# Optimization experiments

Hardware: AMD Instinct MI355X
Metric: run time of the kernel (lower is better)

Reference implementation:

```python
import jax, jax.numpy as jnp
import numpy as np

MAX_WORDS = 2048  # max word tokens per sequence (static num_segments)


def setup_inputs() -> dict:
    key = jax.random.key(0)
    k1, k2, k3, k4 = jax.random.split(key, 4)
    B, S, H, D = 8, 4096, 768, 1024
    embeddings = jax.random.normal(k1, (B, S, H), dtype=jnp.float32)
    proj_w = jax.random.normal(k2, (H, D), dtype=jnp.float32) * 0.02
    proj_b = jax.random.normal(k3, (D,), dtype=jnp.float32) * 0.02
    masks = jnp.ones((B, S), dtype=jnp.int32)
    word_ids = jnp.sort(jax.random.randint(k4, (B, S), 0, MAX_WORDS), axis=-1)
    return {"embeddings": embeddings, "proj_w": proj_w, "proj_b": proj_b,
            "masks": masks, "word_ids": word_ids}


def reference(embeddings, proj_w, proj_b, masks, word_ids):
    B, S, H = embeddings.shape
    W = MAX_WORDS
    # Flatten batch+word into one segment id space: seg in [0, B*W)
    seg = (word_ids + jnp.arange(B, dtype=word_ids.dtype)[:, None] * W).reshape(-1)
    flat_emb = embeddings.reshape(B * S, H)
    # segment-sum of embeddings over subwords of each word  -> (B, W, H)
    sum_emb = jax.ops.segment_sum(flat_emb, seg, num_segments=B * W).reshape(B, W, H)
    ones = jnp.ones((B * S,), dtype=jnp.float32)
    counts = jax.ops.segment_sum(ones, seg, num_segments=B * W).reshape(B, W)
    mcounts = jax.ops.segment_sum(masks.reshape(-1).astype(jnp.float32), seg,
                                  num_segments=B * W).reshape(B, W)
    # word is valid iff it has >=1 subword and ALL its subwords have mask==1
    valid = (counts > 0) & (counts == mcounts)
    mean_emb = sum_emb / jnp.maximum(counts, 1.0)[..., None]
    token_embeddings = jnp.where(valid[..., None], mean_emb, 0.0)  # (B, W, H)
    token_masks = valid.astype(jnp.int32)                          # (B, W)
    # projection: hidden 768 -> config.hidden_size 1024
    out = jnp.einsum('bwh,hd->bwd', token_embeddings, proj_w) + proj_b
    return out, token_masks
```

## Files before the change

### kernel.cpp

```cpp
#include <hip/hip_runtime.h>
#include <hip/hip_bf16.h>
#include <stdint.h>

#define Bn 8
#define Sn 4096
#define Hn 768
#define Dn 1024
#define Wn 2048

typedef __attribute__((ext_vector_type(8))) short short8;
typedef __attribute__((ext_vector_type(4))) short short4v;
typedef __attribute__((ext_vector_type(4))) float floatx4;

__device__ __forceinline__ void load_lds16(const void* g, void* l) {
  __builtin_amdgcn_global_load_lds(
      (const __attribute__((address_space(1))) void*)g,
      (__attribute__((address_space(3))) void*)l, 16, 0, 0);
}

__global__ __launch_bounds__(256) void k_prep(const float* __restrict__ pw,
                                              const int* __restrict__ wid,
                                              __hip_bfloat16* __restrict__ wb,
                                              int* __restrict__ starts) {
  if (blockIdx.x < 768) {
    __shared__ float tile[32][33];
    const int bt = blockIdx.x;
    const int d0 = (bt % 32) * 32, h0 = (bt / 32) * 32;
    const int tx = threadIdx.x & 31, ty = threadIdx.x >> 5;
#pragma unroll
    for (int i = 0; i < 32; i += 8)
      tile[ty + i][tx] = pw[(size_t)(h0 + ty + i) * Dn + d0 + tx];
    __syncthreads();
#pragma unroll
    for (int i = 0; i < 32; i += 8)
      wb[(size_t)(d0 + ty + i) * Hn + h0 + tx] = (__hip_bfloat16)tile[tx][ty + i];
  } else {
    const int bid = blockIdx.x - 768;
    const int g = bid * 256 + threadIdx.x;
    const int b = g >> 12, s = g & (Sn - 1);
    const int* wbi = wid + (size_t)b * Sn;
    int* sb = starts + b * (Wn + 1);
    const int cur = wbi[s];
    const int prev = (s == 0) ? -1 : wbi[s - 1];
    for (int ww = prev + 1; ww <= cur; ++ww) sb[ww] = s;
    if (s == Sn - 1)
      for (int ww = cur + 1; ww <= Wn; ++ww) sb[ww] = Sn;
  }
}

__global__ __launch_bounds__(256) void k_words(const float* __restrict__ emb,
                                               const int* __restrict__ masks,
                                               const int* __restrict__ starts,
                                               __hip_bfloat16* __restrict__ wa,
                                               float* __restrict__ out_masks) {
  const int b = blockIdx.y;
  const int wave = threadIdx.x >> 6, lane = threadIdx.x & 63;
  const int w = blockIdx.x * 4 + wave;

  const int* sb = starts + b * (Wn + 1);
  const int start = sb[w];
  const int end = sb[w + 1];
  const int count = end - start;

  const int* mb = masks + (size_t)b * Sn;
  bool allone = true;
  for (int s0 = start; s0 < end; s0 += 64) {
    const int idx = s0 + lane;
    allone = allone && ((idx < end) ? (mb[idx] == 1) : true);
  }
  const bool valid = (count > 0) && __all(allone);
  const float inv = valid ? 1.0f / (float)count : 0.0f;

  floatx4 sum[3] = {{0.f, 0.f, 0.f, 0.f}, {0.f, 0.f, 0.f, 0.f}, {0.f, 0.f, 0.f, 0.f}};
  const float* eb = emb + (size_t)b * Sn * Hn;
  int s = start;
  for (; s + 1 < end; s += 2) {
    const floatx4* r0 = (const floatx4*)(eb + (size_t)s * Hn);
    const floatx4* r1 = (const floatx4*)(eb + (size_t)(s + 1) * Hn);
#pragma unroll
    for (int j = 0; j < 3; ++j) sum[j] += r0[j * 64 + lane];
#pragma unroll
    for (int j = 0; j < 3; ++j) sum[j] += r1[j * 64 + lane];
  }
  if (s < end) {
    const floatx4* r0 = (const floatx4*)(eb + (size_t)s * Hn);
#pragma unroll
    for (int j = 0; j < 3; ++j) sum[j] += r0[j * 64 + lane];
  }

  const size_t rowbase = ((size_t)b * Wn + w) * Hn;
#pragma unroll
  for (int j = 0; j < 3; ++j) {
    short4v o;
#pragma unroll
    for (int c = 0; c < 4; ++c) {
      __hip_bfloat16 h = (__hip_bfloat16)(sum[j][c] * inv);
      o[c] = *reinterpret_cast<short*>(&h);
    }
    *(short4v*)&wa[rowbase + (size_t)(j * 64 + lane) * 4] = o;
  }
  if (lane == 0) out_masks[(size_t)b * Wn + w] = valid ? 1.0f : 0.0f;
}

__global__ __launch_bounds__(256) void k_gemm(const short* __restrict__ A,
                                              const short* __restrict__ Bt,
                                              const float* __restrict__ bias,
                                              float* __restrict__ out) {
  constexpr int K = Hn;
  constexpr int N = Dn;
  __shared__ __align__(16) short lsA[2][128 * 32];
  __shared__ __align__(16) short lsB[2][128 * 32];

  const int t = threadIdx.x;
  const int lane = t & 63, wave = t >> 6;
  const int wm = wave >> 1, wn = wave & 1;
  const int lane16 = lane & 15, quad = lane >> 4;

  const int linear = blockIdx.x;
  const int xcd = linear & 7;
  const int o = linear >> 3;
  const int m0 = (xcd * 16 + (o >> 3)) * 128;
  const int n0 = (o & 7) * 128;

  const int lrow = t >> 2;
  const int lcol = (t & 3) * 8;
  const short* gA0 = A + (size_t)(m0 + lrow) * K + lcol;
  const short* gB0 = Bt + (size_t)(n0 + lrow) * K + lcol;
  const int loff = lrow * 32 + lcol;

  float bv[4];
#pragma unroll
  for (int ni = 0; ni < 4; ++ni)
    bv[ni] = bias[n0 + wn * 64 + ni * 16 + lane16];

  floatx4 acc[4][4];
#pragma unroll
  for (int i = 0; i < 4; ++i)
#pragma unroll
    for (int j = 0; j < 4; ++j) acc[i][j] = (floatx4){0.f, 0.f, 0.f, 0.f};

  for (int k0 = 0; k0 < K; k0 += 64) {
    load_lds16(gA0 + k0,                    &lsA[0][loff]);
    load_lds16(gA0 + (size_t)64 * K + k0,   &lsA[0][loff + 64 * 32]);
    load_lds16(gA0 + k0 + 32,               &lsA[1][loff]);
    load_lds16(gA0 + (size_t)64 * K + k0 + 32, &lsA[1][loff + 64 * 32]);
    load_lds16(gB0 + k0,                    &lsB[0][loff]);
    load_lds16(gB0 + (size_t)64 * K + k0,   &lsB[0][loff + 64 * 32]);
    load_lds16(gB0 + k0 + 32,               &lsB[1][loff]);
    load_lds16(gB0 + (size_t)64 * K + k0 + 32, &lsB[1][loff + 64 * 32]);
    __syncthreads();

#pragma unroll
    for (int sp = 0; sp < 2; ++sp) {
      short8 af[4], bf[4];
#pragma unroll
      for (int mi = 0; mi < 4; ++mi)
        af[mi] = *(const short8*)&lsA[sp][(wm * 64 + mi * 16 + lane16) * 32 + quad * 8];
#pragma unroll
      for (int ni = 0; ni < 4; ++ni)
        bf[ni] = *(const short8*)&lsB[sp][(wn * 64 + ni * 16 + lane16) * 32 + quad * 8];

#pragma unroll
      for (int mi = 0; mi < 4; ++mi)
#pragma unroll
        for (int ni = 0; ni < 4; ++ni)
          acc[mi][ni] = __builtin_amdgcn_mfma_f32_16x16x32_bf16(af[mi], bf[ni], acc[mi][ni], 0, 0, 0);
    }
    __syncthreads();
  }

#pragma unroll
  for (int mi = 0; mi < 4; ++mi) {
#pragma unroll
    for (int ni = 0; ni < 4; ++ni) {
      const int n = n0 + wn * 64 + ni * 16 + lane16;
#pragma unroll
      for (int r = 0; r < 4; ++r) {
        const int m = m0 + wm * 64 + mi * 16 + quad * 4 + r;
        out[(size_t)m * N + n] = acc[mi][ni][r] + bv[ni];
      }
    }
  }
}

extern "C" void kernel_launch(void* const* d_in, const int* in_sizes, int n_in,
                              void* d_out, int out_size, void* d_ws, size_t ws_size,
                              hipStream_t stream) {
  const float* emb    = (const float*)d_in[0];
  const float* proj_w = (const float*)d_in[1];
  const float* proj_b = (const float*)d_in[2];
  const int*   masks  = (const int*)d_in[3];
  const int*   wid    = (const int*)d_in[4];

  float* out = (float*)d_out;
  float* out_masks = out + (size_t)Bn * Wn * Dn;

  __hip_bfloat16* wb = (__hip_bfloat16*)d_ws;
  __hip_bfloat16* wa = wb + (size_t)Dn * Hn;
  int* starts = (int*)(wa + (size_t)Bn * Wn * Hn);

  k_prep<<<dim3(768 + (Bn * Sn) / 256), 256, 0, stream>>>(proj_w, wid, wb, starts);

  k_words<<<dim3(Wn / 4, Bn), 256, 0, stream>>>(emb, masks, starts, wa, out_masks);

  k_gemm<<<dim3(1024), 256, 0, stream>>>((const short*)wa, (const short*)wb, proj_b, out);
}
```

Measured before the change: 206.9 us.

## Restructure GEMM into 256x128 tiles with triple-buffered swizzled LDS pipeline

Replaces the simple 128x128 double-pass GEMM with a 512-thread, 256x128 tile kernel that keeps a three-slot LDS ring buffer (144 KB dynamic shared memory) and prefetches two K-steps ahead. LDS rows are XOR-swizzled to avoid bank conflicts, and MFMA issue is split into two halves with s_setprio and explicit waitcnt/barriers so global loads overlap compute. The aim is to hide memory latency and raise MFMA utilisation. In exchange, occupancy is limited by the large LDS footprint, the grid halves to 512 blocks, and hand-placed waitcnts make the schedule fragile.

```diff
diff --git a/kernel.cpp b/kernel.cpp
--- a/kernel.cpp
+++ b/kernel.cpp
@@ -102,72 +102,131 @@
   if (lane == 0) out_masks[(size_t)b * Wn + w] = valid ? 1.0f : 0.0f;
 }
 
-__global__ __launch_bounds__(256) void k_gemm(const short* __restrict__ A,
-                                              const short* __restrict__ Bt,
-                                              const float* __restrict__ bias,
-                                              float* __restrict__ out) {
-  constexpr int K = Hn;
-  constexpr int N = Dn;
-  __shared__ __align__(16) short lsA[2][128 * 32];
-  __shared__ __align__(16) short lsB[2][128 * 32];
+constexpr int GK = Hn;
+constexpr int LDS_A = 256 * 64;
+constexpr int LDS_B = 128 * 64;
+constexpr int LDS_T = LDS_A + LDS_B;
+
+__global__ __launch_bounds__(512, 2) void k_gemm(const short* __restrict__ A,
+                                                 const short* __restrict__ Bt,
+                                                 const float* __restrict__ bias,
+                                                 float* __restrict__ out) {
+  extern __shared__ __align__(16) short ls[];
 
   const int t = threadIdx.x;
-  const int lane = t & 63, wave = t >> 6;
+  const int lane = t & 63;
+  const int wave = t >> 6;
   const int wm = wave >> 1, wn = wave & 1;
   const int lane16 = lane & 15, quad = lane >> 4;
+  const int swz = lane16 & 7;
 
   const int linear = blockIdx.x;
   const int xcd = linear & 7;
   const int o = linear >> 3;
-  const int m0 = (xcd * 16 + (o >> 3)) * 128;
+  const int m0 = (xcd * 8 + (o >> 3)) * 256;
   const int n0 = (o & 7) * 128;
 
-  const int lrow = t >> 2;
-  const int lcol = (t & 3) * 8;
-  const short* gA0 = A + (size_t)(m0 + lrow) * K + lcol;
-  const short* gB0 = Bt + (size_t)(n0 + lrow) * K + lcol;
-  const int loff = lrow * 32 + lcol;
+  const int rA = t >> 3;
+  const int ssw = ((t & 7) ^ (rA & 7)) * 8;
+  const short* gAs = A + (size_t)(m0 + rA) * GK + ssw;
+  const short* gBs = Bt + (size_t)(n0 + rA) * GK + ssw;
+
+  auto stage_a3 = [&](int slot, int tt) {
+    short* d = ls + slot * LDS_T + t * 8;
+    const short* g = gAs + tt * 64;
+    load_lds16(g, d);
+    load_lds16(g + (size_t)64 * GK, d + 4096);
+    load_lds16(g + (size_t)128 * GK, d + 8192);
+  };
+  auto stage_b3 = [&](int slot, int tt) {
+    short* d = ls + slot * LDS_T + t * 8;
+    load_lds16(gAs + tt * 64 + (size_t)192 * GK, d + 12288);
+    load_lds16(gBs + tt * 64, d + 16384);
+    load_lds16(gBs + tt * 64 + (size_t)64 * GK, d + 20480);
+  };
+
+  auto ld_af = [&](short8 (&af)[2][2], int mib, const short* bufA) {
+#pragma unroll
+    for (int m2 = 0; m2 < 2; ++m2)
+#pragma unroll
+      for (int ks = 0; ks < 2; ++ks)
+        af[m2][ks] = *(const short8*)&bufA[(wm * 64 + (mib + m2) * 16 + lane16) * 64 +
+                                           ((((ks << 2) | quad) ^ swz) << 3)];
+  };
+  auto ld_bf = [&](short8 (&bf)[4][2], const short* bufB) {
+#pragma unroll
+    for (int ni = 0; ni < 4; ++ni)
+#pragma unroll
+      for (int ks = 0; ks < 2; ++ks)
+        bf[ni][ks] = *(const short8*)&bufB[(wn * 64 + ni * 16 + lane16) * 64 +
+                                           ((((ks << 2) | quad) ^ swz) << 3)];
+  };
+
+  floatx4 acc[4][4];
+#pragma unroll
+  for (int i = 0; i < 4; ++i)
+#pragma unroll
+    for (int j = 0; j < 4; ++j) acc[i][j] = (floatx4){0.f, 0.f, 0.f, 0.f};
+
+  auto mmac2 = [&](short8 (&af)[2][2], short8 (&bf)[4][2], int mib) {
+    __builtin_amdgcn_s_setprio(1);
+#pragma unroll
+    for (int m2 = 0; m2 < 2; ++m2)
+#pragma unroll
+      for (int ni = 0; ni < 4; ++ni)
+#pragma unroll
+        for (int ks = 0; ks < 2; ++ks)
+          acc[mib + m2][ni] = __builtin_amdgcn_mfma_f32_16x16x32_bf16(
+              af[m2][ks], bf[ni][ks], acc[mib + m2][ni], 0, 0, 0);
+    __builtin_amdgcn_s_setprio(0);
+  };
+
+  stage_a3(0, 0);
+  stage_b3(0, 0);
+  stage_a3(1, 1);
+  stage_b3(1, 1);
+  asm volatile("s_waitcnt vmcnt(6)" ::: "memory");
+  __builtin_amdgcn_sched_barrier(0);
+  __builtin_amdgcn_s_barrier();
+
+  int cur = 0;
+#pragma unroll 1
+  for (int tt = 0; tt < 12; ++tt) {
+    const short* bufA = ls + cur * LDS_T;
+    const short* bufB = bufA + LDS_A;
+    const int nx2 = (cur + 2 >= 3) ? cur - 1 : cur + 2;
+    const bool st = tt < 10;
+    short8 af[2][2], bf[4][2];
+
+    ld_af(af, 0, bufA);
+    ld_bf(bf, bufB);
+    if (st) stage_a3(nx2, tt + 2);
+    __builtin_amdgcn_s_barrier();
+    asm volatile("s_waitcnt lgkmcnt(0)" ::: "memory");
+    __builtin_amdgcn_sched_barrier(0);
+    mmac2(af, bf, 0);
+    __builtin_amdgcn_s_barrier();
+
+    ld_af(af, 2, bufA);
+    if (st) stage_b3(nx2, tt + 2);
+    if (tt < 10) {
+      asm volatile("s_waitcnt vmcnt(6)" ::: "memory");
+    } else if (tt == 10) {
+      asm volatile("s_waitcnt vmcnt(0)" ::: "memory");
+    }
+    __builtin_amdgcn_sched_barrier(0);
+    __builtin_amdgcn_s_barrier();
+    asm volatile("s_waitcnt lgkmcnt(0)" ::: "memory");
+    __builtin_amdgcn_sched_barrier(0);
+    mmac2(af, bf, 2);
+    __builtin_amdgcn_s_barrier();
+
+    cur = (cur + 1 == 3) ? 0 : cur + 1;
+  }
 
   float bv[4];
 #pragma unroll
-  for (int ni = 0; ni < 4; ++ni)
-    bv[ni] = bias[n0 + wn * 64 + ni * 16 + lane16];
-
-  floatx4 acc[4][4];
-#pragma unroll
-  for (int i = 0; i < 4; ++i)
-#pragma unroll
-    for (int j = 0; j < 4; ++j) acc[i][j] = (floatx4){0.f, 0.f, 0.f, 0.f};
-
-  for (int k0 = 0; k0 < K; k0 += 64) {
-    load_lds16(gA0 + k0,                    &lsA[0][loff]);
-    load_lds16(gA0 + (size_t)64 * K + k0,   &lsA[0][loff + 64 * 32]);
-    load_lds16(gA0 + k0 + 32,               &lsA[1][loff]);
-    load_lds16(gA0 + (size_t)64 * K + k0 + 32, &lsA[1][loff + 64 * 32]);
-    load_lds16(gB0 + k0,                    &lsB[0][loff]);
-    load_lds16(gB0 + (size_t)64 * K + k0,   &lsB[0][loff + 64 * 32]);
-    load_lds16(gB0 + k0 + 32,               &lsB[1][loff]);
-    load_lds16(gB0 + (size_t)64 * K + k0 + 32, &lsB[1][loff + 64 * 32]);
-    __syncthreads();
-
-#pragma unroll
-    for (int sp = 0; sp < 2; ++sp) {
-      short8 af[4], bf[4];
-#pragma unroll
-      for (int mi = 0; mi < 4; ++mi)
-        af[mi] = *(const short8*)&lsA[sp][(wm * 64 + mi * 16 + lane16) * 32 + quad * 8];
-#pragma unroll
-      for (int ni = 0; ni < 4; ++ni)
-        bf[ni] = *(const short8*)&lsB[sp][(wn * 64 + ni * 16 + lane16) * 32 + quad * 8];
-
-#pragma unroll
-      for (int mi = 0; mi < 4; ++mi)
-#pragma unroll
-        for (int ni = 0; ni < 4; ++ni)
-          acc[mi][ni] = __builtin_amdgcn_mfma_f32_16x16x32_bf16(af[mi], bf[ni], acc[mi][ni], 0, 0, 0);
-    }
-    __syncthreads();
-  }
+  for (int ni = 0; ni < 4; ++ni) bv[ni] = bias[n0 + wn * 64 + ni * 16 + lane16];
 
 #pragma unroll
   for (int mi = 0; mi < 4; ++mi) {
@@ -177,7 +236,7 @@
 #pragma unroll
       for (int r = 0; r < 4; ++r) {
         const int m = m0 + wm * 64 + mi * 16 + quad * 4 + r;
-        out[(size_t)m * N + n] = acc[mi][ni][r] + bv[ni];
+        out[(size_t)m * Dn + n] = acc[mi][ni][r] + bv[ni];
       }
     }
   }
@@ -203,5 +262,10 @@
 
   k_words<<<dim3(Wn / 4, Bn), 256, 0, stream>>>(emb, masks, starts, wa, out_masks);
 
-  k_gemm<<<dim3(1024), 256, 0, stream>>>((const short*)wa, (const short*)wb, proj_b, out);
-}
+  constexpr int kGemmLds = 3 * LDS_T * (int)sizeof(short);
+  static_assert(kGemmLds == 147456, "LDS budget");
+  (void)hipFuncSetAttribute((const void*)k_gemm,
+                            hipFuncAttributeMaxDynamicSharedMemorySize, kGemmLds);
+  k_gemm<<<dim3(512), 512, kGemmLds, stream>>>((const short*)wa, (const short*)wb,
+                                               proj_b, out);
+}
```

Result: no change. 209.9 us (+1.5%).

## Fuse prep and word kernels using wave-level binary search for word bounds

Applied to the files above, without the earlier changes.

Replaces the separate starts-table build and word-averaging kernels with one front kernel. Each wave finds its word's start and end by a two-level ballot/popcount lower-bound search over the sorted word ids, and the weight transpose runs as extra blocks in the same launch. This removes one launch and its dependency, plus the starts buffer round trip. The GEMM output also switches to nontemporal stores to reduce cache pollution. Each wave now does extra index loads for the search.

```diff
diff --git a/kernel.cpp b/kernel.cpp
--- a/kernel.cpp
+++ b/kernel.cpp
@@ -18,13 +18,27 @@
       (__attribute__((address_space(3))) void*)l, 16, 0, 0);
 }
 
-__global__ __launch_bounds__(256) void k_prep(const float* __restrict__ pw,
-                                              const int* __restrict__ wid,
-                                              __hip_bfloat16* __restrict__ wb,
-                                              int* __restrict__ starts) {
-  if (blockIdx.x < 768) {
+__device__ __forceinline__ int lb4096(const int* __restrict__ a, int x, int lane) {
+  const int p = a[lane << 6];
+  const unsigned long long m1 = __ballot(p < x);
+  const int n1 = __popcll(m1);
+  const int base = (n1 > 0 ? n1 - 1 : 0) << 6;
+  const int q = a[base + lane];
+  const unsigned long long m2 = __ballot(q < x);
+  return base + __popcll(m2);
+}
+
+__global__ __launch_bounds__(256) void k_front(const float* __restrict__ emb,
+                                               const float* __restrict__ pw,
+                                               const int* __restrict__ masks,
+                                               const int* __restrict__ wid,
+                                               __hip_bfloat16* __restrict__ wb,
+                                               __hip_bfloat16* __restrict__ wa,
+                                               float* __restrict__ out_masks) {
+  const int bid = blockIdx.x;
+  if (bid >= 4096) {
     __shared__ float tile[32][33];
-    const int bt = blockIdx.x;
+    const int bt = bid - 4096;
     const int d0 = (bt % 32) * 32, h0 = (bt / 32) * 32;
     const int tx = threadIdx.x & 31, ty = threadIdx.x >> 5;
 #pragma unroll
@@ -34,32 +48,16 @@
 #pragma unroll
     for (int i = 0; i < 32; i += 8)
       wb[(size_t)(d0 + ty + i) * Hn + h0 + tx] = (__hip_bfloat16)tile[tx][ty + i];
-  } else {
-    const int bid = blockIdx.x - 768;
-    const int g = bid * 256 + threadIdx.x;
-    const int b = g >> 12, s = g & (Sn - 1);
-    const int* wbi = wid + (size_t)b * Sn;
-    int* sb = starts + b * (Wn + 1);
-    const int cur = wbi[s];
-    const int prev = (s == 0) ? -1 : wbi[s - 1];
-    for (int ww = prev + 1; ww <= cur; ++ww) sb[ww] = s;
-    if (s == Sn - 1)
-      for (int ww = cur + 1; ww <= Wn; ++ww) sb[ww] = Sn;
-  }
-}
-
-__global__ __launch_bounds__(256) void k_words(const float* __restrict__ emb,
-                                               const int* __restrict__ masks,
-                                               const int* __restrict__ starts,
-                                               __hip_bfloat16* __restrict__ wa,
-                                               float* __restrict__ out_masks) {
-  const int b = blockIdx.y;
+    return;
+  }
+
+  const int b = bid >> 9;
   const int wave = threadIdx.x >> 6, lane = threadIdx.x & 63;
-  const int w = blockIdx.x * 4 + wave;
-
-  const int* sb = starts + b * (Wn + 1);
-  const int start = sb[w];
-  const int end = sb[w + 1];
+  const int w = (bid & 511) * 4 + wave;
+
+  const int* wbi = wid + (size_t)b * Sn;
+  const int start = lb4096(wbi, w, lane);
+  const int end = lb4096(wbi, w + 1, lane);
   const int count = end - start;
 
   const int* mb = masks + (size_t)b * Sn;
@@ -177,7 +175,7 @@
 #pragma unroll
       for (int r = 0; r < 4; ++r) {
         const int m = m0 + wm * 64 + mi * 16 + quad * 4 + r;
-        out[(size_t)m * N + n] = acc[mi][ni][r] + bv[ni];
+        __builtin_nontemporal_store(acc[mi][ni][r] + bv[ni], &out[(size_t)m * N + n]);
       }
     }
   }
@@ -197,11 +195,10 @@
 
   __hip_bfloat16* wb = (__hip_bfloat16*)d_ws;
   __hip_bfloat16* wa = wb + (size_t)Dn * Hn;
-  int* starts = (int*)(wa + (size_t)Bn * Wn * Hn);
-
-  k_prep<<<dim3(768 + (Bn * Sn) / 256), 256, 0, stream>>>(proj_w, wid, wb, starts);
-
-  k_words<<<dim3(Wn / 4, Bn), 256, 0, stream>>>(emb, masks, starts, wa, out_masks);
-
-  k_gemm<<<dim3(1024), 256, 0, stream>>>((const short*)wa, (const short*)wb, proj_b, out);
-}
+
+  k_front<<<dim3(4096 + 768), 256, 0, stream>>>(emb, proj_w, masks, wid, wb, wa,
+                                                out_masks);
+
+  k_gemm<<<dim3(1024), 256, 0, stream>>>((const short*)wa, (const short*)wb,
+                                         proj_b, out);
+}
```

Result: slower. 211.7 us (+2.3%).
